# Performance work log

Hardware: AMD Instinct MI355X
Metric: run time of the kernel (lower is better)

## Reference

```python
import jax, jax.numpy as jnp
import numpy as np

H = 128          # hidden_dim
L = 10           # num_iterations
NC = 8000        # check nodes
NV = 16000       # var nodes
E = 60000        # edges per direction
INPUT_SCALE = 0.1
LN_EPS = 1e-6


def _glorot(key, shape):
    fan_in, fan_out = shape[0], shape[-1]
    lim = np.sqrt(6.0 / (fan_in + fan_out))
    return jax.random.uniform(key, shape, jnp.float32, -lim, lim)


def _ln(x, g, b):
    m = jnp.mean(x, axis=-1, keepdims=True)
    v = jnp.var(x, axis=-1, keepdims=True)
    return g * (x - m) / jnp.sqrt(v + LN_EPS) + b


def _gru(x, h, W, U, b):
    # Keras GRUCell, reset_after=True; gate order: z (update), r (reset), h (candidate)
    xa = x @ W + b[0]            # [N, 3H]
    ha = h @ U + b[1]            # [N, 3H]
    z = jax.nn.sigmoid(xa[:, :H] + ha[:, :H])
    r = jax.nn.sigmoid(xa[:, H:2 * H] + ha[:, H:2 * H])
    hh = jnp.tanh(xa[:, 2 * H:] + r * ha[:, 2 * H:])
    return z * h + (1.0 - z) * hh


def setup_inputs() -> dict:
    key = jax.random.key(0)
    ks = jax.random.split(key, 24)
    d = {
        'check_feats': jax.random.normal(ks[0], (NC, 1), jnp.float32),
        'var_feats': jax.random.normal(ks[1], (NV, 1), jnp.float32),
        'c2v_src': jax.random.randint(ks[2], (E,), 0, NC, jnp.int32),
        'c2v_tgt': jax.random.randint(ks[3], (E,), 0, NV, jnp.int32),
        'v2c_src': jax.random.randint(ks[4], (E,), 0, NV, jnp.int32),
        'v2c_tgt': jax.random.randint(ks[5], (E,), 0, NC, jnp.int32),
        # input transforms (Dense 1->H) + LayerNorm params
        'Wc_in': _glorot(ks[6], (1, H)), 'bc_in': jnp.zeros((H,), jnp.float32),
        'Wv_in': _glorot(ks[7], (1, H)), 'bv_in': jnp.zeros((H,), jnp.float32),
        'gc_ln': jnp.ones((H,), jnp.float32), 'bc_ln': jnp.zeros((H,), jnp.float32),
        'gv_ln': jnp.ones((H,), jnp.float32), 'bv_ln': jnp.zeros((H,), jnp.float32),
        # SimpleConv message Dense(2H->H) per receiving node set
        'Wmsg_c': _glorot(ks[8], (2 * H, H)), 'bmsg_c': jnp.zeros((H,), jnp.float32),
        'Wmsg_v': _glorot(ks[9], (2 * H, H)), 'bmsg_v': jnp.zeros((H,), jnp.float32),
        # NextStateFromConcat Dense(2H->H)
        'Wns_c': _glorot(ks[10], (2 * H, H)), 'bns_c': jnp.zeros((H,), jnp.float32),
        'Wns_v': _glorot(ks[11], (2 * H, H)), 'bns_v': jnp.zeros((H,), jnp.float32),
        # GRU cells: kernel [H,3H], recurrent [H,3H], bias [2,3H]
        'Wg_c': _glorot(ks[12], (H, 3 * H)), 'Ug_c': _glorot(ks[13], (H, 3 * H)),
        'bg_c': jnp.zeros((2, 3 * H), jnp.float32),
        'Wg_v': _glorot(ks[14], (H, 3 * H)), 'Ug_v': _glorot(ks[15], (H, 3 * H)),
        'bg_v': jnp.zeros((2, 3 * H), jnp.float32),
        # final predictor Dense(H->1), bias = logit(p_error)
        'Wf': _glorot(ks[16], (H, 1)),
        'bf': jnp.full((1,), np.log((4.0 / NV) / (1 - 4.0 / NV)), jnp.float32),
    }
    return d


def reference(check_feats, var_feats, c2v_src, c2v_tgt, v2c_src, v2c_tgt,
              Wc_in, bc_in, Wv_in, bv_in, gc_ln, bc_ln, gv_ln, bv_ln,
              Wmsg_c, bmsg_c, Wmsg_v, bmsg_v, Wns_c, bns_c, Wns_v, bns_v,
              Wg_c, Ug_c, bg_c, Wg_v, Ug_v, bg_v, Wf, bf):
    hc = _ln((INPUT_SCALE * check_feats) @ Wc_in + bc_in, gc_ln, bc_ln)  # [NC,H]
    hv = _ln((INPUT_SCALE * var_feats) @ Wv_in + bv_in, gv_ln, bv_ln)    # [NV,H]
    for _ in range(L):
        # v_to_c SimpleConv: concat(sender var state, receiver check state) -> Dense+ELU -> scatter-sum
        m_vc = jax.nn.elu(jnp.concatenate([hv[v2c_src], hc[v2c_tgt]], axis=-1) @ Wmsg_c + bmsg_c)
        agg_c = jax.ops.segment_sum(m_vc, v2c_tgt, num_segments=NC)
        # c_to_v SimpleConv
        m_cv = jax.nn.elu(jnp.concatenate([hc[c2v_src], hv[c2v_tgt]], axis=-1) @ Wmsg_v + bmsg_v)
        agg_v = jnp.asarray(jax.ops.segment_sum(m_cv, c2v_tgt, num_segments=NV))
        # NextStateFromConcat: Dense(concat(old_state, pooled)) + ELU
        upd_c = jax.nn.elu(jnp.concatenate([hc, agg_c], axis=-1) @ Wns_c + bns_c)
        upd_v = jax.nn.elu(jnp.concatenate([hv, agg_v], axis=-1) @ Wns_v + bns_v)
        # GRU state update (update info is the input, prev state is the hidden state)
        hc = _gru(upd_c, hc, Wg_c, Ug_c, bg_c)
        hv = _gru(upd_v, hv, Wg_v, Ug_v, bg_v)
    # dropout is identity at inference; final Dense(H->1), squeeze
    return (hv @ Wf + bf)[:, 0]
```

## Files before the change

kernel.cpp:

```cpp
#include <hip/hip_runtime.h>
#include <hip/hip_bf16.h>
#include <math.h>

#define Hdim 128
#define NCn  8000
#define NVn  16000
#define NE   60000
#define LITERS 10
#define NCB16 500
#define NVB16 1000
#define NCB32 250
#define NVB32 500
#define PREPB 1280
#define INITB 6000
#define ZEROB 188
#define FILLB 235

typedef __attribute__((ext_vector_type(8))) short s8v;
typedef __attribute__((ext_vector_type(4))) float f4v;

__device__ __forceinline__ float fexp(float x) { return __expf(x); }
__device__ __forceinline__ float elu_f(float x) { return x > 0.0f ? x : (fexp(x) - 1.0f); }
__device__ __forceinline__ float sigm_f(float x) {
    return __builtin_amdgcn_rcpf(1.0f + fexp(-x));
}
__device__ __forceinline__ float tanh_f(float x) {
    return 1.0f - 2.0f * __builtin_amdgcn_rcpf(1.0f + fexp(2.0f * x));
}
__device__ __forceinline__ unsigned short f2b(float x) {
    __hip_bfloat16 h = __float2bfloat16(x); return *(unsigned short*)&h;
}
__device__ __forceinline__ float b2f(unsigned short u) {
    __hip_bfloat16 h; *(unsigned short*)&h = u; return __bfloat162float(h);
}

__global__ void prep_init(const float* __restrict__ Wmsg_c, const float* __restrict__ Wmsg_v,
                          const float* __restrict__ Wns_c,  const float* __restrict__ Wns_v,
                          const float* __restrict__ Wg_c, const float* __restrict__ Ug_c,
                          const float* __restrict__ Wg_v, const float* __restrict__ Ug_v,
                          unsigned short* __restrict__ Fmsg_c, unsigned short* __restrict__ Fmsg_v,
                          unsigned short* __restrict__ Fns_c,  unsigned short* __restrict__ Fns_v,
                          unsigned short* __restrict__ Fcat_c, unsigned short* __restrict__ Fcat_v,
                          const float* __restrict__ cf, const float* __restrict__ vf,
                          const float* __restrict__ Wc, const float* __restrict__ bc,
                          const float* __restrict__ Wv, const float* __restrict__ bv,
                          const float* __restrict__ gc, const float* __restrict__ bcl,
                          const float* __restrict__ gv, const float* __restrict__ bvl,
                          float* __restrict__ hc, float* __restrict__ hv,
                          int* __restrict__ cnts) {
    if (blockIdx.x >= PREPB + INITB) {
        int i = (blockIdx.x - PREPB - INITB) * 256 + threadIdx.x;
        if (i < 48000) cnts[i] = 0;
        return;
    }
    if (blockIdx.x < PREPB) {
        int idx = blockIdx.x * 256 + threadIdx.x;
        const int S1 = 4 * 32768;
        const int S2 = S1 + 2 * 98304;
        if (idx < S1) {
            int seg = idx >> 15, t = idx & 32767;
            const float* W = (seg == 0) ? Wmsg_c : (seg == 1) ? Wmsg_v : (seg == 2) ? Wns_c : Wns_v;
            unsigned short* outw = (seg == 0) ? Fmsg_c : (seg == 1) ? Fmsg_v : (seg == 2) ? Fns_c : Fns_v;
            int j = t & 7, lane = (t >> 3) & 63, t2 = t >> 9;
            int f = t2 & 7, kt = t2 >> 3;
            int n = f * 16 + (lane & 15), k = kt * 32 + (lane >> 4) * 8 + j;
            outw[t] = f2b(W[(size_t)k * 128 + n]);
        } else if (idx < S2) {
            int q = idx - S1;
            int seg = q / 98304, t = q - seg * 98304;
            const float* Wg = seg ? Wg_v : Wg_c;
            const float* Ug = seg ? Ug_v : Ug_c;
            unsigned short* outw = seg ? Fcat_v : Fcat_c;
            int j = t & 7, lane = (t >> 3) & 63, t2 = t >> 9;
            int f = t2 % 24, kt = t2 / 24;
            int n = f * 16 + (lane & 15), k = kt * 32 + (lane >> 4) * 8 + j;
            outw[t] = f2b((k < 128) ? Ug[(size_t)k * 384 + n] : Wg[(size_t)(k - 128) * 384 + n]);
        }
        return;
    }
    int node = (blockIdx.x - PREPB) * 4 + (threadIdx.x >> 6);
    int lane = threadIdx.x & 63;
    const float *Win, *bin, *g, *bl;
    float f;
    float* outp;
    if (node < NCn) {
        f = cf[node]; Win = Wc; bin = bc; g = gc; bl = bcl;
        outp = hc + (size_t)node * Hdim;
    } else {
        int n2 = node - NCn;
        f = vf[n2]; Win = Wv; bin = bv; g = gv; bl = bvl;
        outp = hv + (size_t)n2 * Hdim;
    }
    f *= 0.1f;
    float x0 = f * Win[lane] + bin[lane];
    float x1 = f * Win[lane + 64] + bin[lane + 64];
    float s = x0 + x1;
    float sq = x0 * x0 + x1 * x1;
    #pragma unroll
    for (int off = 32; off > 0; off >>= 1) {
        s += __shfl_xor(s, off);
        sq += __shfl_xor(sq, off);
    }
    float m = s * (1.0f / 128.0f);
    float v = sq * (1.0f / 128.0f) - m * m;
    float inv = 1.0f / sqrtf(v + 1e-6f);
    outp[lane]      = g[lane]      * (x0 - m) * inv + bl[lane];
    outp[lane + 64] = g[lane + 64] * (x1 - m) * inv + bl[lane + 64];
}

__global__ void hist_kernel(const int* __restrict__ tgt_c, const int* __restrict__ tgt_v,
                            int* __restrict__ cnt_c, int* __restrict__ cnt_v) {
    int e = blockIdx.x * blockDim.x + threadIdx.x;
    if (e >= NE) return;
    atomicAdd(&cnt_c[tgt_c[e]], 1);
    atomicAdd(&cnt_v[tgt_v[e]], 1);
}
__launch_bounds__(1024)
__global__ void scan2_kernel(const int* __restrict__ cnt_c, int* __restrict__ rp_c,
                             const int* __restrict__ cnt_v, int* __restrict__ rp_v) {
    const int* cnt = blockIdx.x ? cnt_v : cnt_c;
    int* rowptr = blockIdx.x ? rp_v : rp_c;
    const int n = blockIdx.x ? NVn : NCn;
    __shared__ int part[1024];
    int t = threadIdx.x;
    int chunk = (n + 1023) >> 10;
    int base = t * chunk;
    int s = 0;
    for (int i = 0; i < chunk; i++) { int idx = base + i; if (idx < n) s += cnt[idx]; }
    part[t] = s;
    __syncthreads();
    for (int off = 1; off < 1024; off <<= 1) {
        int u = (t >= off) ? part[t - off] : 0;
        __syncthreads();
        part[t] += u;
        __syncthreads();
    }
    int run = part[t] - s;
    for (int i = 0; i < chunk; i++) {
        int idx = base + i;
        if (idx < n) { rowptr[idx] = run; run += cnt[idx]; }
    }
    if (t == 0) rowptr[n] = part[1023];
}

__launch_bounds__(256)
__global__ void fill_pq(const int* __restrict__ tgt_c, const int* __restrict__ tgt_v,
                        const int* __restrict__ src_c, const int* __restrict__ src_v,
                        const int* __restrict__ rp_c, const int* __restrict__ rp_v,
                        int* __restrict__ fill_c, int* __restrict__ fill_v,
                        int* __restrict__ srcs_c, int* __restrict__ srcs_v,
                        const float* __restrict__ hc, const float* __restrict__ hv,
                        const unsigned short* __restrict__ Fmsg_c, const unsigned short* __restrict__ Fmsg_v,
                        const float* __restrict__ bmsg_c, const float* __restrict__ bmsg_v,
                        unsigned short* __restrict__ Pv_w, unsigned short* __restrict__ Qc_w,
                        unsigned short* __restrict__ Pc_w, unsigned short* __restrict__ Qv_w) {
    if (blockIdx.x < FILLB) {
        int e = blockIdx.x * 256 + threadIdx.x;
        if (e >= NE) return;
        int tc = tgt_c[e];
        srcs_c[rp_c[tc] + atomicAdd(&fill_c[tc], 1)] = src_c[e];
        int tv = tgt_v[e];
        srcs_v[rp_v[tv] + atomicAdd(&fill_v[tv], 1)] = src_v[e];
        return;
    }
    __shared__ unsigned short sA[32 * 136];
    const int bid = blockIdx.x - FILLB;
    const int isV = (bid >= NCB32) ? 1 : 0;
    const int blockM = (isV ? (bid - NCB32) : bid) * 32;
    const float* h = isV ? hv : hc;
    const unsigned short* FP = isV ? Fmsg_c : Fmsg_v;
    const unsigned short* FQ = isV ? Fmsg_v : Fmsg_c;
    const float* bq = isV ? bmsg_v : bmsg_c;
    unsigned short* Pw = isV ? Pv_w : Pc_w;
    unsigned short* Qw = isV ? Qv_w : Qc_w;

    const int tid = threadIdx.x;
    const int lane = tid & 63, wave = tid >> 6;
    const int quad = lane >> 4, l16 = lane & 15;
    {
        int rr = tid >> 3, cc = tid & 7;
        const float* hrow = &h[(size_t)(blockM + rr) * Hdim + cc * 16];
        f4v x0 = *(const f4v*)hrow;
        f4v x1 = *(const f4v*)(hrow + 4);
        f4v x2 = *(const f4v*)(hrow + 8);
        f4v x3 = *(const f4v*)(hrow + 12);
        s8v w0, w1;
        #pragma unroll
        for (int i = 0; i < 4; i++) {
            w0[i] = (short)f2b(x0[i]); w0[i + 4] = (short)f2b(x1[i]);
            w1[i] = (short)f2b(x2[i]); w1[i + 4] = (short)f2b(x3[i]);
        }
        *(s8v*)&sA[rr * 136 + cc * 16]     = w0;
        *(s8v*)&sA[rr * 136 + cc * 16 + 8] = w1;
    }
    __syncthreads();

    f4v accP[2][2], accQ[2][2];
    #pragma unroll
    for (int mt = 0; mt < 2; mt++)
        #pragma unroll
        for (int u = 0; u < 2; u++) { accP[mt][u] = (f4v){0.f,0.f,0.f,0.f}; accQ[mt][u] = (f4v){0.f,0.f,0.f,0.f}; }

    #pragma unroll
    for (int kt = 0; kt < 4; kt++) {
        s8v a0 = *(const s8v*)&sA[l16 * 136 + kt * 32 + quad * 8];
        s8v a1 = *(const s8v*)&sA[(16 + l16) * 136 + kt * 32 + quad * 8];
        #pragma unroll
        for (int u = 0; u < 2; u++) {
            int ct = wave * 2 + u;
            s8v bp = *(const s8v*)&FP[((size_t)(kt * 8 + ct) * 64 + lane) * 8];
            s8v bqv = *(const s8v*)&FQ[((size_t)((kt + 4) * 8 + ct) * 64 + lane) * 8];
            accP[0][u] = __builtin_amdgcn_mfma_f32_16x16x32_bf16(a0, bp, accP[0][u], 0, 0, 0);
            accP[1][u] = __builtin_amdgcn_mfma_f32_16x16x32_bf16(a1, bp, accP[1][u], 0, 0, 0);
            accQ[0][u] = __builtin_amdgcn_mfma_f32_16x16x32_bf16(a0, bqv, accQ[0][u], 0, 0, 0);
            accQ[1][u] = __builtin_amdgcn_mfma_f32_16x16x32_bf16(a1, bqv, accQ[1][u], 0, 0, 0);
        }
    }
    #pragma unroll
    for (int u = 0; u < 2; u++) {
        int col = (wave * 2 + u) * 16 + l16;
        float qbias = bq[col];
        #pragma unroll
        for (int mt = 0; mt < 2; mt++)
            #pragma unroll
            for (int reg = 0; reg < 4; reg++) {
                int row = blockM + mt * 16 + quad * 4 + reg;
                Pw[(size_t)row * Hdim + col] = f2b(accP[mt][u][reg]);
                Qw[(size_t)row * Hdim + col] = f2b(accQ[mt][u][reg] + qbias);
            }
    }
}

__launch_bounds__(256)
__global__ void node_fused(float* __restrict__ hc, float* __restrict__ hv,
                           const int* __restrict__ rp_c, const int* __restrict__ rp_v,
                           const int* __restrict__ srcs_c, const int* __restrict__ srcs_v,
                           const unsigned short* __restrict__ Pv_r, const unsigned short* __restrict__ Qc_r,
                           const unsigned short* __restrict__ Pc_r, const unsigned short* __restrict__ Qv_r,
                           unsigned short* __restrict__ Pv_w, unsigned short* __restrict__ Qc_w,
                           unsigned short* __restrict__ Pc_w, unsigned short* __restrict__ Qv_w,
                           const unsigned short* __restrict__ Fns_c, const float* __restrict__ bns_c,
                           const unsigned short* __restrict__ Fns_v, const float* __restrict__ bns_v,
                           const unsigned short* __restrict__ Fcat_c, const unsigned short* __restrict__ Fcat_v,
                           const float* __restrict__ bg_c, const float* __restrict__ bg_v,
                           const unsigned short* __restrict__ Fmsg_c, const unsigned short* __restrict__ Fmsg_v,
                           const float* __restrict__ bmsg_c, const float* __restrict__ bmsg_v,
                           const float* __restrict__ Wf, const float* __restrict__ bf,
                           float* __restrict__ out, int do_pq, int vOnly) {
    __shared__ unsigned short sA[16 * 264];
    __shared__ unsigned short sU[16 * 136];
    __shared__ float sHf[16 * 128];
    __shared__ float sRed[64];
    const int bid = blockIdx.x;
    const int isV = vOnly ? 1 : ((bid >= NCB16) ? 1 : 0);
    const int blockM = (vOnly ? bid : (isV ? (bid - NCB16) : bid)) * 16;
    float* h = isV ? hv : hc;
    const int* rp = isV ? rp_v : rp_c;
    const int* srcs = isV ? srcs_v : srcs_c;
    const unsigned short* Pr = isV ? Pc_r : Pv_r;
    const unsigned short* Qr = isV ? Qv_r : Qc_r;
    const unsigned short* Fns = isV ? Fns_v : Fns_c;
    const float* bns = isV ? bns_v : bns_c;
    const unsigned short* Fcat = isV ? Fcat_v : Fcat_c;
    const float* bg = isV ? bg_v : bg_c;
    const unsigned short* FP = isV ? Fmsg_c : Fmsg_v;
    const unsigned short* FQ = isV ? Fmsg_v : Fmsg_c;
    const float* bq = isV ? bmsg_v : bmsg_c;
    unsigned short* Pw = isV ? Pv_w : Pc_w;
    unsigned short* Qw = isV ? Qv_w : Qc_w;

    const int tid = threadIdx.x;
    const int lane = tid & 63, wave = tid >> 6;
    const int quad = lane >> 4, l16 = lane & 15;
    const int r = tid >> 4, ch = tid & 15;
    const int node = blockM + r;

    {
        s8v q8 = *(const s8v*)&Qr[(size_t)node * Hdim + ch * 8];
        const float* hrow = &h[(size_t)node * Hdim + ch * 8];
        f4v h0 = *(const f4v*)hrow;
        f4v h1 = *(const f4v*)(hrow + 4);
        int j = rp[node];
        const int e0 = rp[node + 1];

        s8v hw;
        #pragma unroll
        for (int i = 0; i < 4; i++) { hw[i] = (short)f2b(h0[i]); hw[i + 4] = (short)f2b(h1[i]); }
        *(s8v*)&sA[r * 264 + ch * 8] = hw;
        *(f4v*)&sHf[r * 128 + ch * 8]     = h0;
        *(f4v*)&sHf[r * 128 + ch * 8 + 4] = h1;

        float qf[8], acc[8];
        #pragma unroll
        for (int i = 0; i < 8; i++) { qf[i] = b2f((unsigned short)q8[i]); acc[i] = 0.0f; }

        for (; j + 8 <= e0; j += 8) {
            s8v p[8];
            #pragma unroll
            for (int b = 0; b < 8; b++)
                p[b] = *(const s8v*)&Pr[(size_t)srcs[j + b] * Hdim + ch * 8];
            #pragma unroll
            for (int b = 0; b < 8; b++)
                #pragma unroll
                for (int i = 0; i < 8; i++) acc[i] += elu_f(b2f((unsigned short)p[b][i]) + qf[i]);
        }
        if (j + 4 <= e0) {
            s8v p[4];
            #pragma unroll
            for (int b = 0; b < 4; b++)
                p[b] = *(const s8v*)&Pr[(size_t)srcs[j + b] * Hdim + ch * 8];
            #pragma unroll
            for (int b = 0; b < 4; b++)
                #pragma unroll
                for (int i = 0; i < 8; i++) acc[i] += elu_f(b2f((unsigned short)p[b][i]) + qf[i]);
            j += 4;
        }
        if (j + 2 <= e0) {
            s8v p0 = *(const s8v*)&Pr[(size_t)srcs[j] * Hdim + ch * 8];
            s8v p1 = *(const s8v*)&Pr[(size_t)srcs[j + 1] * Hdim + ch * 8];
            #pragma unroll
            for (int i = 0; i < 8; i++) acc[i] += elu_f(b2f((unsigned short)p0[i]) + qf[i]);
            #pragma unroll
            for (int i = 0; i < 8; i++) acc[i] += elu_f(b2f((unsigned short)p1[i]) + qf[i]);
            j += 2;
        }
        if (j < e0) {
            s8v p0 = *(const s8v*)&Pr[(size_t)srcs[j] * Hdim + ch * 8];
            #pragma unroll
            for (int i = 0; i < 8; i++) acc[i] += elu_f(b2f((unsigned short)p0[i]) + qf[i]);
        }
        s8v w;
        #pragma unroll
        for (int i = 0; i < 8; i++) w[i] = (short)f2b(acc[i]);
        *(s8v*)&sA[r * 264 + 128 + ch * 8] = w;
    }
    __syncthreads();

    f4v accA[2];
    accA[0] = (f4v){0.f,0.f,0.f,0.f};
    accA[1] = (f4v){0.f,0.f,0.f,0.f};
    #pragma unroll
    for (int kt = 0; kt < 8; kt++) {
        s8v a = *(const s8v*)&sA[l16 * 264 + kt * 32 + quad * 8];
        #pragma unroll
        for (int u = 0; u < 2; u++) {
            s8v b = *(const s8v*)&Fns[((size_t)(kt * 8 + wave * 2 + u) * 64 + lane) * 8];
            accA[u] = __builtin_amdgcn_mfma_f32_16x16x32_bf16(a, b, accA[u], 0, 0, 0);
        }
    }
    #pragma unroll
    for (int u = 0; u < 2; u++) {
        int col = (wave * 2 + u) * 16 + l16;
        float bb = bns[col];
        #pragma unroll
        for (int reg = 0; reg < 4; reg++)
            sU[(quad * 4 + reg) * 136 + col] = f2b(elu_f(accA[u][reg] + bb));
    }
    __syncthreads();

    float hnv[2][4];
    #pragma unroll
    for (int u = 0; u < 2; u++) {
        const int j = wave * 2 + u;
        f4v sZ = (f4v){0.f,0.f,0.f,0.f};
        f4v sR = (f4v){0.f,0.f,0.f,0.f};
        f4v sH1 = (f4v){0.f,0.f,0.f,0.f};
        f4v sH2 = (f4v){0.f,0.f,0.f,0.f};
        #pragma unroll
        for (int kt = 0; kt < 8; kt++) {
            s8v a = (kt < 4)
                ? *(const s8v*)&sA[l16 * 264 + kt * 32 + quad * 8]
                : *(const s8v*)&sU[l16 * 136 + (kt - 4) * 32 + quad * 8];
            s8v bz = *(const s8v*)&Fcat[((size_t)(kt * 24 + j) * 64 + lane) * 8];
            s8v br = *(const s8v*)&Fcat[((size_t)(kt * 24 + 8 + j) * 64 + lane) * 8];
            s8v bh = *(const s8v*)&Fcat[((size_t)(kt * 24 + 16 + j) * 64 + lane) * 8];
            sZ = __builtin_amdgcn_mfma_f32_16x16x32_bf16(a, bz, sZ, 0, 0, 0);
            sR = __builtin_amdgcn_mfma_f32_16x16x32_bf16(a, br, sR, 0, 0, 0);
            if (kt < 4)
                sH1 = __builtin_amdgcn_mfma_f32_16x16x32_bf16(a, bh, sH1, 0, 0, 0);
            else
                sH2 = __builtin_amdgcn_mfma_f32_16x16x32_bf16(a, bh, sH2, 0, 0, 0);
        }
        const int t = j * 16 + l16;
        float bz2 = bg[t]       + bg[384 + t];
        float br2 = bg[128 + t] + bg[512 + t];
        float b0h = bg[256 + t];
        float b1h = bg[640 + t];
        #pragma unroll
        for (int reg = 0; reg < 4; reg++) {
            int rloc = quad * 4 + reg;
            float z = sigm_f(sZ[reg] + sH1[reg] * 0.0f + bz2 + 0.0f);
            z = sigm_f(sZ[reg] + bz2);
            float rr = sigm_f(sR[reg] + br2);
            float hh = tanh_f((sH2[reg] + b0h) + rr * (sH1[reg] + b1h));
            float hold = sHf[rloc * 128 + t];
            float hn = z * hold + (1.0f - z) * hh;
            if (do_pq) h[(size_t)(blockM + rloc) * Hdim + t] = hn;
            hnv[u][reg] = hn;
        }
    }

    if (!do_pq) {
        float wf0 = Wf[(wave * 2 + 0) * 16 + l16];
        float wf1 = Wf[(wave * 2 + 1) * 16 + l16];
        float part[4];
        #pragma unroll
        for (int reg = 0; reg < 4; reg++)
            part[reg] = hnv[0][reg] * wf0 + hnv[1][reg] * wf1;
        #pragma unroll
        for (int off = 1; off < 16; off <<= 1) {
            #pragma unroll
            for (int reg = 0; reg < 4; reg++)
                part[reg] += __shfl_xor(part[reg], off);
        }
        if (l16 == 0) {
            #pragma unroll
            for (int reg = 0; reg < 4; reg++)
                sRed[wave * 16 + quad * 4 + reg] = part[reg];
        }
        __syncthreads();
        if (tid < 16)
            out[blockM + tid] = sRed[tid] + sRed[16 + tid] + sRed[32 + tid] + sRed[48 + tid] + bf[0];
        return;
    }

    __syncthreads();
    #pragma unroll
    for (int u = 0; u < 2; u++) {
        int col = (wave * 2 + u) * 16 + l16;
        #pragma unroll
        for (int reg = 0; reg < 4; reg++)
            sA[(quad * 4 + reg) * 264 + col] = f2b(hnv[u][reg]);
    }
    __syncthreads();

    f4v accP[2], accQ[2];
    accP[0] = (f4v){0.f,0.f,0.f,0.f}; accP[1] = (f4v){0.f,0.f,0.f,0.f};
    accQ[0] = (f4v){0.f,0.f,0.f,0.f}; accQ[1] = (f4v){0.f,0.f,0.f,0.f};
    #pragma unroll
    for (int kt = 0; kt < 4; kt++) {
        s8v a = *(const s8v*)&sA[l16 * 264 + kt * 32 + quad * 8];
        #pragma unroll
        for (int u = 0; u < 2; u++) {
            int ct = wave * 2 + u;
            s8v bp = *(const s8v*)&FP[((size_t)(kt * 8 + ct) * 64 + lane) * 8];
            s8v bqv = *(const s8v*)&FQ[((size_t)((kt + 4) * 8 + ct) * 64 + lane) * 8];
            accP[u] = __builtin_amdgcn_mfma_f32_16x16x32_bf16(a, bp, accP[u], 0, 0, 0);
            accQ[u] = __builtin_amdgcn_mfma_f32_16x16x32_bf16(a, bqv, accQ[u], 0, 0, 0);
        }
    }
    #pragma unroll
    for (int u = 0; u < 2; u++) {
        int col = (wave * 2 + u) * 16 + l16;
        float qbias = bq[col];
        #pragma unroll
        for (int reg = 0; reg < 4; reg++) {
            int row = blockM + quad * 4 + reg;
            Pw[(size_t)row * Hdim + col] = f2b(accP[u][reg]);
            Qw[(size_t)row * Hdim + col] = f2b(accQ[u][reg] + qbias);
        }
    }
}

extern "C" void kernel_launch(void* const* d_in, const int* in_sizes, int n_in,
                              void* d_out, int out_size, void* d_ws, size_t ws_size,
                              hipStream_t stream) {
    const float* cf      = (const float*)d_in[0];
    const float* vf      = (const float*)d_in[1];
    const int*   c2v_src = (const int*)d_in[2];
    const int*   c2v_tgt = (const int*)d_in[3];
    const int*   v2c_src = (const int*)d_in[4];
    const int*   v2c_tgt = (const int*)d_in[5];
    const float* Wc_in   = (const float*)d_in[6];
    const float* bc_in   = (const float*)d_in[7];
    const float* Wv_in   = (const float*)d_in[8];
    const float* bv_in   = (const float*)d_in[9];
    const float* gc_ln   = (const float*)d_in[10];
    const float* bc_ln   = (const float*)d_in[11];
    const float* gv_ln   = (const float*)d_in[12];
    const float* bv_ln   = (const float*)d_in[13];
    const float* Wmsg_c  = (const float*)d_in[14];
    const float* bmsg_c  = (const float*)d_in[15];
    const float* Wmsg_v  = (const float*)d_in[16];
    const float* bmsg_v  = (const float*)d_in[17];
    const float* Wns_c   = (const float*)d_in[18];
    const float* bns_c   = (const float*)d_in[19];
    const float* Wns_v   = (const float*)d_in[20];
    const float* bns_v   = (const float*)d_in[21];
    const float* Wg_c    = (const float*)d_in[22];
    const float* Ug_c    = (const float*)d_in[23];
    const float* bg_c    = (const float*)d_in[24];
    const float* Wg_v    = (const float*)d_in[25];
    const float* Ug_v    = (const float*)d_in[26];
    const float* bg_v    = (const float*)d_in[27];
    const float* Wf      = (const float*)d_in[28];
    const float* bf      = (const float*)d_in[29];
    float* out = (float*)d_out;

    char* p = (char*)d_ws;
    #define CARVE(name, type, count) type* name = (type*)p; p += (((size_t)(count) * sizeof(type)) + 255) & ~(size_t)255;
    CARVE(hc,     float, NCn * Hdim)
    CARVE(hv,     float, NVn * Hdim)
    CARVE(Pv0,    unsigned short, NVn * Hdim)
    CARVE(Qc0,    unsigned short, NCn * Hdim)
    CARVE(Pc0,    unsigned short, NCn * Hdim)
    CARVE(Qv0,    unsigned short, NVn * Hdim)
    CARVE(Pv1,    unsigned short, NVn * Hdim)
    CARVE(Qc1,    unsigned short, NCn * Hdim)
    CARVE(Pc1,    unsigned short, NCn * Hdim)
    CARVE(Qv1,    unsigned short, NVn * Hdim)
    CARVE(Fmsg_c, unsigned short, 32768)
    CARVE(Fmsg_v, unsigned short, 32768)
    CARVE(Fns_c,  unsigned short, 32768)
    CARVE(Fns_v,  unsigned short, 32768)
    CARVE(Fcat_c, unsigned short, 98304)
    CARVE(Fcat_v, unsigned short, 98304)
    CARVE(rp_c,  int, NCn + 8)
    CARVE(rp_v,  int, NVn + 8)
    CARVE(srcs_c, int, NE)
    CARVE(srcs_v, int, NE)
    CARVE(cnts,  int, 48000)
    #undef CARVE
    int* cnt_c  = cnts;
    int* cnt_v  = cnts + NCn;
    int* fill_c = cnts + NCn + NVn;
    int* fill_v = cnts + 2 * NCn + NVn;

    prep_init<<<PREPB + INITB + ZEROB, 256, 0, stream>>>(
        Wmsg_c, Wmsg_v, Wns_c, Wns_v, Wg_c, Ug_c, Wg_v, Ug_v,
        Fmsg_c, Fmsg_v, Fns_c, Fns_v, Fcat_c, Fcat_v,
        cf, vf, Wc_in, bc_in, Wv_in, bv_in, gc_ln, bc_ln, gv_ln, bv_ln, hc, hv, cnts);
    hist_kernel<<<(NE + 255) / 256, 256, 0, stream>>>(v2c_tgt, c2v_tgt, cnt_c, cnt_v);
    scan2_kernel<<<2, 1024, 0, stream>>>(cnt_c, rp_c, cnt_v, rp_v);
    fill_pq<<<FILLB + NCB32 + NVB32, 256, 0, stream>>>(
        v2c_tgt, c2v_tgt, v2c_src, c2v_src, rp_c, rp_v, fill_c, fill_v, srcs_c, srcs_v,
        hc, hv, Fmsg_c, Fmsg_v, bmsg_c, bmsg_v, Pv0, Qc0, Pc0, Qv0);

    unsigned short* Pv_[2] = {Pv0, Pv1};
    unsigned short* Qc_[2] = {Qc0, Qc1};
    unsigned short* Pc_[2] = {Pc0, Pc1};
    unsigned short* Qv_[2] = {Qv0, Qv1};

    for (int it = 0; it < LITERS; it++) {
        int rd = it & 1, wr = rd ^ 1;
        int last = (it == LITERS - 1);
        node_fused<<<last ? NVB16 : (NCB16 + NVB16), 256, 0, stream>>>(
            hc, hv, rp_c, rp_v, srcs_c, srcs_v,
            Pv_[rd], Qc_[rd], Pc_[rd], Qv_[rd],
            Pv_[wr], Qc_[wr], Pc_[wr], Qv_[wr],
            Fns_c, bns_c, Fns_v, bns_v,
            Fcat_c, Fcat_v, bg_c, bg_v,
            Fmsg_c, Fmsg_v, bmsg_c, bmsg_v,
            Wf, bf, out, last ? 0 : 1, last ? 1 : 0);
    }
}
```

Before: 499.7 us.

## Process 32 nodes per block to reuse weight fragments across two M-tiles

The fused node kernel now handles 32 rows per block instead of 16, so each weight B-fragment loaded from global memory feeds two MFMA tiles, halving weight traffic per node. The gather phase gives each thread 16 channels instead of 8 and unrolls by 4 edges instead of 8. This doubles LDS use and accumulator registers, and halves the grid to 750 blocks, which may reduce occupancy and latency hiding in the irregular gather.

```diff
diff --git a/kernel.cpp b/kernel.cpp
--- a/kernel.cpp
+++ b/kernel.cpp
@@ -7,8 +7,6 @@
 #define NVn  16000
 #define NE   60000
 #define LITERS 10
-#define NCB16 500
-#define NVB16 1000
 #define NCB32 250
 #define NVB32 500
 #define PREPB 1280
@@ -247,13 +245,13 @@
                            const float* __restrict__ bmsg_c, const float* __restrict__ bmsg_v,
                            const float* __restrict__ Wf, const float* __restrict__ bf,
                            float* __restrict__ out, int do_pq, int vOnly) {
-    __shared__ unsigned short sA[16 * 264];
-    __shared__ unsigned short sU[16 * 136];
-    __shared__ float sHf[16 * 128];
-    __shared__ float sRed[64];
+    __shared__ unsigned short sA[32 * 264];
+    __shared__ unsigned short sU[32 * 136];
+    __shared__ float sHf[32 * 128];
+    __shared__ float sRed[4][32];
     const int bid = blockIdx.x;
-    const int isV = vOnly ? 1 : ((bid >= NCB16) ? 1 : 0);
-    const int blockM = (vOnly ? bid : (isV ? (bid - NCB16) : bid)) * 16;
+    const int isV = vOnly ? 1 : ((bid >= NCB32) ? 1 : 0);
+    const int blockM = (vOnly ? bid : (isV ? (bid - NCB32) : bid)) * 32;
     float* h = isV ? hv : hc;
     const int* rp = isV ? rp_v : rp_c;
     const int* srcs = isV ? srcs_v : srcs_c;
@@ -272,80 +270,105 @@
     const int tid = threadIdx.x;
     const int lane = tid & 63, wave = tid >> 6;
     const int quad = lane >> 4, l16 = lane & 15;
-    const int r = tid >> 4, ch = tid & 15;
+    const int r = tid >> 3, ch = tid & 7;
     const int node = blockM + r;
 
     {
-        s8v q8 = *(const s8v*)&Qr[(size_t)node * Hdim + ch * 8];
-        const float* hrow = &h[(size_t)node * Hdim + ch * 8];
+        const int cb = ch * 16;
+        s8v q8a = *(const s8v*)&Qr[(size_t)node * Hdim + cb];
+        s8v q8b = *(const s8v*)&Qr[(size_t)node * Hdim + cb + 8];
+        const float* hrow = &h[(size_t)node * Hdim + cb];
         f4v h0 = *(const f4v*)hrow;
         f4v h1 = *(const f4v*)(hrow + 4);
+        f4v h2 = *(const f4v*)(hrow + 8);
+        f4v h3 = *(const f4v*)(hrow + 12);
         int j = rp[node];
         const int e0 = rp[node + 1];
 
-        s8v hw;
-        #pragma unroll
-        for (int i = 0; i < 4; i++) { hw[i] = (short)f2b(h0[i]); hw[i + 4] = (short)f2b(h1[i]); }
-        *(s8v*)&sA[r * 264 + ch * 8] = hw;
-        *(f4v*)&sHf[r * 128 + ch * 8]     = h0;
-        *(f4v*)&sHf[r * 128 + ch * 8 + 4] = h1;
-
-        float qf[8], acc[8];
-        #pragma unroll
-        for (int i = 0; i < 8; i++) { qf[i] = b2f((unsigned short)q8[i]); acc[i] = 0.0f; }
-
-        for (; j + 8 <= e0; j += 8) {
-            s8v p[8];
-            #pragma unroll
-            for (int b = 0; b < 8; b++)
-                p[b] = *(const s8v*)&Pr[(size_t)srcs[j + b] * Hdim + ch * 8];
-            #pragma unroll
-            for (int b = 0; b < 8; b++)
+        s8v hw0, hw1;
+        #pragma unroll
+        for (int i = 0; i < 4; i++) {
+            hw0[i] = (short)f2b(h0[i]); hw0[i + 4] = (short)f2b(h1[i]);
+            hw1[i] = (short)f2b(h2[i]); hw1[i + 4] = (short)f2b(h3[i]);
+        }
+        *(s8v*)&sA[r * 264 + cb]     = hw0;
+        *(s8v*)&sA[r * 264 + cb + 8] = hw1;
+        *(f4v*)&sHf[r * 128 + cb]      = h0;
+        *(f4v*)&sHf[r * 128 + cb + 4]  = h1;
+        *(f4v*)&sHf[r * 128 + cb + 8]  = h2;
+        *(f4v*)&sHf[r * 128 + cb + 12] = h3;
+
+        float qf[16], acc[16];
+        #pragma unroll
+        for (int i = 0; i < 8; i++) {
+            qf[i]     = b2f((unsigned short)q8a[i]); acc[i]     = 0.0f;
+            qf[i + 8] = b2f((unsigned short)q8b[i]); acc[i + 8] = 0.0f;
+        }
+
+        for (; j + 4 <= e0; j += 4) {
+            s8v pa[4], pb[4];
+            #pragma unroll
+            for (int b = 0; b < 4; b++) {
+                const unsigned short* pr = &Pr[(size_t)srcs[j + b] * Hdim + cb];
+                pa[b] = *(const s8v*)pr;
+                pb[b] = *(const s8v*)(pr + 8);
+            }
+            #pragma unroll
+            for (int b = 0; b < 4; b++) {
                 #pragma unroll
-                for (int i = 0; i < 8; i++) acc[i] += elu_f(b2f((unsigned short)p[b][i]) + qf[i]);
-        }
-        if (j + 4 <= e0) {
-            s8v p[4];
-            #pragma unroll
-            for (int b = 0; b < 4; b++)
-                p[b] = *(const s8v*)&Pr[(size_t)srcs[j + b] * Hdim + ch * 8];
-            #pragma unroll
-            for (int b = 0; b < 4; b++)
+                for (int i = 0; i < 8; i++) acc[i]     += elu_f(b2f((unsigned short)pa[b][i]) + qf[i]);
                 #pragma unroll
-                for (int i = 0; i < 8; i++) acc[i] += elu_f(b2f((unsigned short)p[b][i]) + qf[i]);
-            j += 4;
+                for (int i = 0; i < 8; i++) acc[i + 8] += elu_f(b2f((unsigned short)pb[b][i]) + qf[i + 8]);
+            }
         }
         if (j + 2 <= e0) {
-            s8v p0 = *(const s8v*)&Pr[(size_t)srcs[j] * Hdim + ch * 8];
-            s8v p1 = *(const s8v*)&Pr[(size_t)srcs[j + 1] * Hdim + ch * 8];
-            #pragma unroll
-            for (int i = 0; i < 8; i++) acc[i] += elu_f(b2f((unsigned short)p0[i]) + qf[i]);
-            #pragma unroll
-            for (int i = 0; i < 8; i++) acc[i] += elu_f(b2f((unsigned short)p1[i]) + qf[i]);
+            s8v pa[2], pb[2];
+            #pragma unroll
+            for (int b = 0; b < 2; b++) {
+                const unsigned short* pr = &Pr[(size_t)srcs[j + b] * Hdim + cb];
+                pa[b] = *(const s8v*)pr;
+                pb[b] = *(const s8v*)(pr + 8);
+            }
+            #pragma unroll
+            for (int b = 0; b < 2; b++) {
+                #pragma unroll
+                for (int i = 0; i < 8; i++) acc[i]     += elu_f(b2f((unsigned short)pa[b][i]) + qf[i]);
+                #pragma unroll
+                for (int i = 0; i < 8; i++) acc[i + 8] += elu_f(b2f((unsigned short)pb[b][i]) + qf[i + 8]);
+            }
             j += 2;
         }
         if (j < e0) {
-            s8v p0 = *(const s8v*)&Pr[(size_t)srcs[j] * Hdim + ch * 8];
-            #pragma unroll
-            for (int i = 0; i < 8; i++) acc[i] += elu_f(b2f((unsigned short)p0[i]) + qf[i]);
-        }
-        s8v w;
-        #pragma unroll
-        for (int i = 0; i < 8; i++) w[i] = (short)f2b(acc[i]);
-        *(s8v*)&sA[r * 264 + 128 + ch * 8] = w;
+            const unsigned short* pr = &Pr[(size_t)srcs[j] * Hdim + cb];
+            s8v pa = *(const s8v*)pr;
+            s8v pb = *(const s8v*)(pr + 8);
+            #pragma unroll
+            for (int i = 0; i < 8; i++) acc[i]     += elu_f(b2f((unsigned short)pa[i]) + qf[i]);
+            #pragma unroll
+            for (int i = 0; i < 8; i++) acc[i + 8] += elu_f(b2f((unsigned short)pb[i]) + qf[i + 8]);
+        }
+        s8v w0, w1;
+        #pragma unroll
+        for (int i = 0; i < 8; i++) { w0[i] = (short)f2b(acc[i]); w1[i] = (short)f2b(acc[i + 8]); }
+        *(s8v*)&sA[r * 264 + 128 + cb]     = w0;
+        *(s8v*)&sA[r * 264 + 128 + cb + 8] = w1;
     }
     __syncthreads();
 
-    f4v accA[2];
-    accA[0] = (f4v){0.f,0.f,0.f,0.f};
-    accA[1] = (f4v){0.f,0.f,0.f,0.f};
+    f4v accA[2][2];
+    #pragma unroll
+    for (int mt = 0; mt < 2; mt++)
+        #pragma unroll
+        for (int u = 0; u < 2; u++) accA[mt][u] = (f4v){0.f,0.f,0.f,0.f};
     #pragma unroll
     for (int kt = 0; kt < 8; kt++) {
-        s8v a = *(const s8v*)&sA[l16 * 264 + kt * 32 + quad * 8];
+        s8v a0 = *(const s8v*)&sA[l16 * 264 + kt * 32 + quad * 8];
+        s8v a1 = *(const s8v*)&sA[(16 + l16) * 264 + kt * 32 + quad * 8];
         #pragma unroll
         for (int u = 0; u < 2; u++) {
             s8v b = *(const s8v*)&Fns[((size_t)(kt * 8 + wave * 2 + u) * 64 + lane) * 8];
-            accA[u] = __builtin_amdgcn_mfma_f32_16x16x32_bf16(a, b, accA[u], 0, 0, 0);
+            accA[0][u] = __builtin_amdgcn_mfma_f32_16x16x32_bf16(a0, b, accA[0][u], 0, 0, 0);
+            accA[1][u] = __builtin_amdgcn_mfma_f32_16x16x32_bf16(a1, b, accA[1][u], 0, 0, 0);
         }
     }
     #pragma unroll
@@ -353,33 +376,47 @@
         int col = (wave * 2 + u) * 16 + l16;
         float bb = bns[col];
         #pragma unroll
-        for (int reg = 0; reg < 4; reg++)
-            sU[(quad * 4 + reg) * 136 + col] = f2b(elu_f(accA[u][reg] + bb));
+        for (int mt = 0; mt < 2; mt++)
+            #pragma unroll
+            for (int reg = 0; reg < 4; reg++)
+                sU[(mt * 16 + quad * 4 + reg) * 136 + col] = f2b(elu_f(accA[mt][u][reg] + bb));
     }
     __syncthreads();
 
-    float hnv[2][4];
+    float hnv[2][2][4];
     #pragma unroll
     for (int u = 0; u < 2; u++) {
         const int j = wave * 2 + u;
-        f4v sZ = (f4v){0.f,0.f,0.f,0.f};
-        f4v sR = (f4v){0.f,0.f,0.f,0.f};
-        f4v sH1 = (f4v){0.f,0.f,0.f,0.f};
-        f4v sH2 = (f4v){0.f,0.f,0.f,0.f};
+        f4v sZ[2], sR[2], sH1[2], sH2[2];
+        #pragma unroll
+        for (int mt = 0; mt < 2; mt++) {
+            sZ[mt] = (f4v){0.f,0.f,0.f,0.f}; sR[mt] = (f4v){0.f,0.f,0.f,0.f};
+            sH1[mt] = (f4v){0.f,0.f,0.f,0.f}; sH2[mt] = (f4v){0.f,0.f,0.f,0.f};
+        }
         #pragma unroll
         for (int kt = 0; kt < 8; kt++) {
-            s8v a = (kt < 4)
-                ? *(const s8v*)&sA[l16 * 264 + kt * 32 + quad * 8]
-                : *(const s8v*)&sU[l16 * 136 + (kt - 4) * 32 + quad * 8];
+            s8v a0, a1;
+            if (kt < 4) {
+                a0 = *(const s8v*)&sA[l16 * 264 + kt * 32 + quad * 8];
+                a1 = *(const s8v*)&sA[(16 + l16) * 264 + kt * 32 + quad * 8];
+            } else {
+                a0 = *(const s8v*)&sU[l16 * 136 + (kt - 4) * 32 + quad * 8];
+                a1 = *(const s8v*)&sU[(16 + l16) * 136 + (kt - 4) * 32 + quad * 8];
+            }
             s8v bz = *(const s8v*)&Fcat[((size_t)(kt * 24 + j) * 64 + lane) * 8];
             s8v br = *(const s8v*)&Fcat[((size_t)(kt * 24 + 8 + j) * 64 + lane) * 8];
             s8v bh = *(const s8v*)&Fcat[((size_t)(kt * 24 + 16 + j) * 64 + lane) * 8];
-            sZ = __builtin_amdgcn_mfma_f32_16x16x32_bf16(a, bz, sZ, 0, 0, 0);
-            sR = __builtin_amdgcn_mfma_f32_16x16x32_bf16(a, br, sR, 0, 0, 0);
-            if (kt < 4)
-                sH1 = __builtin_amdgcn_mfma_f32_16x16x32_bf16(a, bh, sH1, 0, 0, 0);
-            else
-                sH2 = __builtin_amdgcn_mfma_f32_16x16x32_bf16(a, bh, sH2, 0, 0, 0);
+            sZ[0] = __builtin_amdgcn_mfma_f32_16x16x32_bf16(a0, bz, sZ[0], 0, 0, 0);
+            sZ[1] = __builtin_amdgcn_mfma_f32_16x16x32_bf16(a1, bz, sZ[1], 0, 0, 0);
+            sR[0] = __builtin_amdgcn_mfma_f32_16x16x32_bf16(a0, br, sR[0], 0, 0, 0);
+            sR[1] = __builtin_amdgcn_mfma_f32_16x16x32_bf16(a1, br, sR[1], 0, 0, 0);
+            if (kt < 4) {
+                sH1[0] = __builtin_amdgcn_mfma_f32_16x16x32_bf16(a0, bh, sH1[0], 0, 0, 0);
+                sH1[1] = __builtin_amdgcn_mfma_f32_16x16x32_bf16(a1, bh, sH1[1], 0, 0, 0);
+            } else {
+                sH2[0] = __builtin_amdgcn_mfma_f32_16x16x32_bf16(a0, bh, sH2[0], 0, 0, 0);
+                sH2[1] = __builtin_amdgcn_mfma_f32_16x16x32_bf16(a1, bh, sH2[1], 0, 0, 0);
+            }
         }
         const int t = j * 16 + l16;
         float bz2 = bg[t]       + bg[384 + t];
@@ -387,40 +424,47 @@
         float b0h = bg[256 + t];
         float b1h = bg[640 + t];
         #pragma unroll
-        for (int reg = 0; reg < 4; reg++) {
-            int rloc = quad * 4 + reg;
-            float z = sigm_f(sZ[reg] + sH1[reg] * 0.0f + bz2 + 0.0f);
-            z = sigm_f(sZ[reg] + bz2);
-            float rr = sigm_f(sR[reg] + br2);
-            float hh = tanh_f((sH2[reg] + b0h) + rr * (sH1[reg] + b1h));
-            float hold = sHf[rloc * 128 + t];
-            float hn = z * hold + (1.0f - z) * hh;
-            if (do_pq) h[(size_t)(blockM + rloc) * Hdim + t] = hn;
-            hnv[u][reg] = hn;
-        }
+        for (int mt = 0; mt < 2; mt++)
+            #pragma unroll
+            for (int reg = 0; reg < 4; reg++) {
+                int rloc = mt * 16 + quad * 4 + reg;
+                float z = sigm_f(sZ[mt][reg] + bz2);
+                float rr = sigm_f(sR[mt][reg] + br2);
+                float hh = tanh_f((sH2[mt][reg] + b0h) + rr * (sH1[mt][reg] + b1h));
+                float hold = sHf[rloc * 128 + t];
+                float hn = z * hold + (1.0f - z) * hh;
+                if (do_pq) h[(size_t)(blockM + rloc) * Hdim + t] = hn;
+                hnv[u][mt][reg] = hn;
+            }
     }
 
     if (!do_pq) {
         float wf0 = Wf[(wave * 2 + 0) * 16 + l16];
         float wf1 = Wf[(wave * 2 + 1) * 16 + l16];
-        float part[4];
-        #pragma unroll
-        for (int reg = 0; reg < 4; reg++)
-            part[reg] = hnv[0][reg] * wf0 + hnv[1][reg] * wf1;
+        float part[2][4];
+        #pragma unroll
+        for (int mt = 0; mt < 2; mt++)
+            #pragma unroll
+            for (int reg = 0; reg < 4; reg++)
+                part[mt][reg] = hnv[0][mt][reg] * wf0 + hnv[1][mt][reg] * wf1;
         #pragma unroll
         for (int off = 1; off < 16; off <<= 1) {
             #pragma unroll
-            for (int reg = 0; reg < 4; reg++)
-                part[reg] += __shfl_xor(part[reg], off);
+            for (int mt = 0; mt < 2; mt++)
+                #pragma unroll
+                for (int reg = 0; reg < 4; reg++)
+                    part[mt][reg] += __shfl_xor(part[mt][reg], off);
         }
         if (l16 == 0) {
             #pragma unroll
-            for (int reg = 0; reg < 4; reg++)
-                sRed[wave * 16 + quad * 4 + reg] = part[reg];
+            for (int mt = 0; mt < 2; mt++)
+                #pragma unroll
+                for (int reg = 0; reg < 4; reg++)
+                    sRed[wave][mt * 16 + quad * 4 + reg] = part[mt][reg];
         }
         __syncthreads();
-        if (tid < 16)
-            out[blockM + tid] = sRed[tid] + sRed[16 + tid] + sRed[32 + tid] + sRed[48 + tid] + bf[0];
+        if (tid < 32)
+            out[blockM + tid] = sRed[0][tid] + sRed[1][tid] + sRed[2][tid] + sRed[3][tid] + bf[0];
         return;
     }
 
@@ -429,24 +473,31 @@
     for (int u = 0; u < 2; u++) {
         int col = (wave * 2 + u) * 16 + l16;
         #pragma unroll
-        for (int reg = 0; reg < 4; reg++)
-            sA[(quad * 4 + reg) * 264 + col] = f2b(hnv[u][reg]);
+        for (int mt = 0; mt < 2; mt++)
+            #pragma unroll
+            for (int reg = 0; reg < 4; reg++)
+                sA[(mt * 16 + quad * 4 + reg) * 264 + col] = f2b(hnv[u][mt][reg]);
     }
     __syncthreads();
 
-    f4v accP[2], accQ[2];
-    accP[0] = (f4v){0.f,0.f,0.f,0.f}; accP[1] = (f4v){0.f,0.f,0.f,0.f};
-    accQ[0] = (f4v){0.f,0.f,0.f,0.f}; accQ[1] = (f4v){0.f,0.f,0.f,0.f};
+    f4v accP[2][2], accQ[2][2];
+    #pragma unroll
+    for (int mt = 0; mt < 2; mt++)
+        #pragma unroll
+        for (int u = 0; u < 2; u++) { accP[mt][u] = (f4v){0.f,0.f,0.f,0.f}; accQ[mt][u] = (f4v){0.f,0.f,0.f,0.f}; }
     #pragma unroll
     for (int kt = 0; kt < 4; kt++) {
-        s8v a = *(const s8v*)&sA[l16 * 264 + kt * 32 + quad * 8];
+        s8v a0 = *(const s8v*)&sA[l16 * 264 + kt * 32 + quad * 8];
+        s8v a1 = *(const s8v*)&sA[(16 + l16) * 264 + kt * 32 + quad * 8];
         #pragma unroll
         for (int u = 0; u < 2; u++) {
             int ct = wave * 2 + u;
             s8v bp = *(const s8v*)&FP[((size_t)(kt * 8 + ct) * 64 + lane) * 8];
             s8v bqv = *(const s8v*)&FQ[((size_t)((kt + 4) * 8 + ct) * 64 + lane) * 8];
-            accP[u] = __builtin_amdgcn_mfma_f32_16x16x32_bf16(a, bp, accP[u], 0, 0, 0);
-            accQ[u] = __builtin_amdgcn_mfma_f32_16x16x32_bf16(a, bqv, accQ[u], 0, 0, 0);
+            accP[0][u] = __builtin_amdgcn_mfma_f32_16x16x32_bf16(a0, bp, accP[0][u], 0, 0, 0);
+            accP[1][u] = __builtin_amdgcn_mfma_f32_16x16x32_bf16(a1, bp, accP[1][u], 0, 0, 0);
+            accQ[0][u] = __builtin_amdgcn_mfma_f32_16x16x32_bf16(a0, bqv, accQ[0][u], 0, 0, 0);
+            accQ[1][u] = __builtin_amdgcn_mfma_f32_16x16x32_bf16(a1, bqv, accQ[1][u], 0, 0, 0);
         }
     }
     #pragma unroll
@@ -454,11 +505,13 @@
         int col = (wave * 2 + u) * 16 + l16;
         float qbias = bq[col];
         #pragma unroll
-        for (int reg = 0; reg < 4; reg++) {
-            int row = blockM + quad * 4 + reg;
-            Pw[(size_t)row * Hdim + col] = f2b(accP[u][reg]);
-            Qw[(size_t)row * Hdim + col] = f2b(accQ[u][reg] + qbias);
-        }
+        for (int mt = 0; mt < 2; mt++)
+            #pragma unroll
+            for (int reg = 0; reg < 4; reg++) {
+                int row = blockM + mt * 16 + quad * 4 + reg;
+                Pw[(size_t)row * Hdim + col] = f2b(accP[mt][u][reg]);
+                Qw[(size_t)row * Hdim + col] = f2b(accQ[mt][u][reg] + qbias);
+            }
     }
 }
 
@@ -544,7 +597,7 @@
     for (int it = 0; it < LITERS; it++) {
         int rd = it & 1, wr = rd ^ 1;
         int last = (it == LITERS - 1);
-        node_fused<<<last ? NVB16 : (NCB16 + NVB16), 256, 0, stream>>>(
+        node_fused<<<last ? NVB32 : (NCB32 + NVB32), 256, 0, stream>>>(
             hc, hv, rp_c, rp_v, srcs_c, srcs_v,
             Pv_[rd], Qc_[rd], Pc_[rd], Qv_[rd],
             Pv_[wr], Qc_[wr], Pc_[wr], Qv_[wr],
```

Result: slower. 576.0 us (+15.3%).
